# Performance work log

Hardware: AMD Instinct MI355X
Metric: run time of the kernel (lower is better)

## Reference

```python
import jax, jax.numpy as jnp
import numpy as np

R = 8921.0  # r defaults to n_labels[0] since args.r <= 0


def setup_inputs() -> dict:
    key = jax.random.key(0)
    k1, k2, k3 = jax.random.split(key, 3)
    B, S, D = 4, 4096, 512
    L = 8921  # n_labels (MIMIC-III full code set)
    x = jax.random.normal(k1, (B, S, D), dtype=jnp.float32)
    # Linear weights initialized N(0, 0.03) as in _init_weights
    W1 = jax.random.normal(k2, (D, D), dtype=jnp.float32) * 0.03  # first_linears[0]: size -> d_a
    W2 = jax.random.normal(k3, (L, D), dtype=jnp.float32) * 0.03  # second_linears[0]: d_a -> n_labels
    return {"x": x, "W1": W1, "W2": W2}


def reference(x, W1, W2):
    # weights = tanh(first_linear(x)) : [B, S, d_a]
    weights = jnp.tanh(jnp.einsum("bsd,ad->bsa", x, W1))
    # att scores: [B, S, L]; softmax over sequence dim (dim=1)
    att = jax.nn.softmax(jnp.einsum("bsa,la->bsl", weights, W2), axis=1)
    att_weights = jnp.swapaxes(att, 1, 2)  # [B, L, S]
    # weighted_output = att_weights @ x : [B, L, D]
    weighted = jnp.einsum("bls,bsd->bld", att_weights, x)
    # non-label attention_mode branch: sum over label dim / r
    out = jnp.sum(weighted, axis=1) / R  # [B, D]
    return (out, att_weights)
```

## Files before the change

kernel.cpp:

```cpp
#include <hip/hip_runtime.h>
#include <stdint.h>

typedef unsigned short u16;
typedef __bf16 bf16x8 __attribute__((ext_vector_type(8)));
typedef float f32x4 __attribute__((ext_vector_type(4)));

#define S_DIM 4096
#define D_DIM 512
#define B_DIM 4
#define L_DIM 8921
#define LPAD  8960
#define M1    16384

__device__ __forceinline__ u16 f2bf(float f) {
  uint32_t u = __float_as_uint(f);
  u += 0x7FFFu + ((u >> 16) & 1u);
  return (u16)(u >> 16);
}
__device__ __forceinline__ float bf2f(u16 u) {
  return __uint_as_float(((uint32_t)u) << 16);
}
__device__ __forceinline__ void async16(const u16* g, u16* l) {
  __builtin_amdgcn_global_load_lds((const __attribute__((address_space(1))) void*)g,
                                   (__attribute__((address_space(3))) void*)l, 16, 0, 0);
}

__global__ __launch_bounds__(256) void cast_pad_kernel(const float* __restrict__ src,
                                                       u16* __restrict__ dst,
                                                       long long nsrc, long long ndst) {
  long long i = ((long long)blockIdx.x * 256 + threadIdx.x) * 4;
  if (i >= ndst) return;
  ushort4 o;
  if (i < nsrc) {
    float4 v = *(const float4*)(src + i);
    o.x = f2bf(v.x); o.y = f2bf(v.y); o.z = f2bf(v.z); o.w = f2bf(v.w);
  } else {
    o.x = 0; o.y = 0; o.z = 0; o.w = 0;
  }
  *(ushort4*)(dst + i) = o;
}

__device__ __forceinline__ void gemm_core(const u16* __restrict__ A, const u16* __restrict__ B,
                                          int tileM, int tileN, u16* Al, u16* Bl,
                                          f32x4 acc[4][4], int waveM, int waveN,
                                          int quad, int l16) {
  const int t = threadIdx.x;
  const int r0 = t >> 2, c0 = (t & 3) * 8;
  for (int k0 = 0; k0 < D_DIM; k0 += 32) {
    async16(A + (size_t)(tileM + r0) * D_DIM + k0 + c0,        Al + t * 8);
    async16(A + (size_t)(tileM + r0 + 64) * D_DIM + k0 + c0,   Al + (t + 256) * 8);
    async16(B + (size_t)(tileN + r0) * D_DIM + k0 + c0,        Bl + t * 8);
    async16(B + (size_t)(tileN + r0 + 64) * D_DIM + k0 + c0,   Bl + (t + 256) * 8);
    __syncthreads();
    bf16x8 af[4], bfr[4];
#pragma unroll
    for (int mi = 0; mi < 4; ++mi)
      af[mi] = *(const bf16x8*)&Al[(waveM + mi * 16 + l16) * 32 + quad * 8];
#pragma unroll
    for (int ni = 0; ni < 4; ++ni)
      bfr[ni] = *(const bf16x8*)&Bl[(waveN + ni * 16 + l16) * 32 + quad * 8];
#pragma unroll
    for (int mi = 0; mi < 4; ++mi)
#pragma unroll
      for (int ni = 0; ni < 4; ++ni)
        acc[mi][ni] = __builtin_amdgcn_mfma_f32_16x16x32_bf16(af[mi], bfr[ni], acc[mi][ni], 0, 0, 0);
    __syncthreads();
  }
}

__global__ __launch_bounds__(256) void gemm1_tanh(const u16* __restrict__ A,
                                                  const u16* __restrict__ B,
                                                  u16* __restrict__ C) {
  __shared__ __align__(16) u16 Al[128 * 32];
  __shared__ __align__(16) u16 Bl[128 * 32];
  const int t = threadIdx.x, lane = t & 63, wave = t >> 6;
  const int quad = lane >> 4, l16 = lane & 15;
  const int tileM = blockIdx.y * 128, tileN = blockIdx.x * 128;
  const int waveM = (wave >> 1) * 64, waveN = (wave & 1) * 64;
  f32x4 acc[4][4];
  const f32x4 z = {0.f, 0.f, 0.f, 0.f};
#pragma unroll
  for (int mi = 0; mi < 4; ++mi)
#pragma unroll
    for (int ni = 0; ni < 4; ++ni) acc[mi][ni] = z;
  gemm_core(A, B, tileM, tileN, Al, Bl, acc, waveM, waveN, quad, l16);
#pragma unroll
  for (int mi = 0; mi < 4; ++mi) {
    const int m0 = tileM + waveM + mi * 16 + quad * 4;
#pragma unroll
    for (int ni = 0; ni < 4; ++ni) {
      const int n = tileN + waveN + ni * 16 + l16;
#pragma unroll
      for (int r = 0; r < 4; ++r)
        C[(size_t)(m0 + r) * D_DIM + n] = f2bf(tanhf(acc[mi][ni][r]));
    }
  }
}

template <bool BF16WS>
__global__ __launch_bounds__(256) void gemm2_exp(const u16* __restrict__ A,
                                                 const u16* __restrict__ Ball,
                                                 u16* __restrict__ scores,
                                                 float* __restrict__ attout,
                                                 float* __restrict__ rowsum) {
  __shared__ __align__(16) u16 Al[128 * 32];
  __shared__ __align__(16) u16 Bl[128 * 32];
  const int b = blockIdx.z;
  const u16* B = Ball + (size_t)b * S_DIM * D_DIM;
  const int t = threadIdx.x, lane = t & 63, wave = t >> 6;
  const int quad = lane >> 4, l16 = lane & 15;
  const int tileM = blockIdx.y * 128, tileN = blockIdx.x * 128;
  const int waveM = (wave >> 1) * 64, waveN = (wave & 1) * 64;
  f32x4 acc[4][4];
  const f32x4 z = {0.f, 0.f, 0.f, 0.f};
#pragma unroll
  for (int mi = 0; mi < 4; ++mi)
#pragma unroll
    for (int ni = 0; ni < 4; ++ni) acc[mi][ni] = z;
  gemm_core(A, B, tileM, tileN, Al, Bl, acc, waveM, waveN, quad, l16);

#pragma unroll
  for (int mi = 0; mi < 4; ++mi) {
    const int l0 = tileM + waveM + mi * 16 + quad * 4;
    float rs[4] = {0.f, 0.f, 0.f, 0.f};
#pragma unroll
    for (int ni = 0; ni < 4; ++ni) {
      const int s = tileN + waveN + ni * 16 + l16;
#pragma unroll
      for (int r = 0; r < 4; ++r) {
        const float ev = __expf(acc[mi][ni][r]);
        rs[r] += ev;
        const int l = l0 + r;
        if (l < L_DIM) {
          const size_t off = ((size_t)b * L_DIM + l) * S_DIM + s;
          if (BF16WS) scores[off] = f2bf(ev);
          else        attout[off] = ev;
        }
      }
    }
#pragma unroll
    for (int r = 0; r < 4; ++r) {
      float v = rs[r];
      v += __shfl_xor(v, 1);
      v += __shfl_xor(v, 2);
      v += __shfl_xor(v, 4);
      v += __shfl_xor(v, 8);
      if (l16 == 0) atomicAdd(&rowsum[(size_t)b * LPAD + l0 + r], v);
    }
  }
}

template <bool BF16WS>
__global__ __launch_bounds__(256) void normalize_colsum(const u16* __restrict__ scores,
                                                        const float* __restrict__ rowsum,
                                                        float* __restrict__ att,
                                                        float* __restrict__ colsum) {
  const int b = blockIdx.y;
  const int l0 = blockIdx.x * 32;
  const int t = threadIdx.x;
  __shared__ float sc[32];
  if (t < 32) {
    const int l = l0 + t;
    sc[t] = (l < L_DIM) ? 1.0f / rowsum[(size_t)b * LPAD + l] : 0.0f;
  }
  __syncthreads();
#pragma unroll
  for (int p = 0; p < 4; ++p) {
    const int s = p * 1024 + t * 4;
    float c0 = 0.f, c1 = 0.f, c2 = 0.f, c3 = 0.f;
    for (int i = 0; i < 32; ++i) {
      const int l = l0 + i;
      if (l >= L_DIM) break;
      const size_t off = ((size_t)b * L_DIM + l) * S_DIM + s;
      const float scale = sc[i];
      float v0, v1, v2, v3;
      if (BF16WS) {
        ushort4 u = *(const ushort4*)(scores + off);
        v0 = bf2f(u.x) * scale; v1 = bf2f(u.y) * scale;
        v2 = bf2f(u.z) * scale; v3 = bf2f(u.w) * scale;
      } else {
        float4 u = *(const float4*)(att + off);
        v0 = u.x * scale; v1 = u.y * scale; v2 = u.z * scale; v3 = u.w * scale;
      }
      float4 o = {v0, v1, v2, v3};
      *(float4*)(att + off) = o;
      c0 += v0; c1 += v1; c2 += v2; c3 += v3;
    }
    float* cs = colsum + (size_t)b * S_DIM + s;
    atomicAdd(cs + 0, c0); atomicAdd(cs + 1, c1);
    atomicAdd(cs + 2, c2); atomicAdd(cs + 3, c3);
  }
}

__global__ __launch_bounds__(256) void out_kernel(const float* __restrict__ x,
                                                  const float* __restrict__ colsum,
                                                  float* __restrict__ out) {
  const int b = blockIdx.y, s0 = blockIdx.x * 128, t = threadIdx.x;
  float a0 = 0.f, a1 = 0.f;
  for (int i = 0; i < 128; ++i) {
    const int s = s0 + i;
    const float c = colsum[(size_t)b * S_DIM + s];
    const float* xr = x + ((size_t)b * S_DIM + s) * D_DIM;
    a0 += c * xr[t];
    a1 += c * xr[t + 256];
  }
  const float invR = 1.0f / 8921.0f;
  atomicAdd(out + b * D_DIM + t,       a0 * invR);
  atomicAdd(out + b * D_DIM + t + 256, a1 * invR);
}

extern "C" void kernel_launch(void* const* d_in, const int* in_sizes, int n_in,
                              void* d_out, int out_size, void* d_ws, size_t ws_size,
                              hipStream_t stream) {
  const float* x  = (const float*)d_in[0];
  const float* W1 = (const float*)d_in[1];
  const float* W2 = (const float*)d_in[2];
  float* out = (float*)d_out;
  float* att = out + 2048;

  char* ws = (char*)d_ws;
  u16*   x_bf   = (u16*)(ws + 0);
  u16*   wt_bf  = (u16*)(ws + 16777216);
  u16*   w1_bf  = (u16*)(ws + 33554432);
  u16*   w2_bf  = (u16*)(ws + 34078720);
  float* rowsum = (float*)(ws + 43253760);
  float* colsum = (float*)(ws + 43397120);
  u16*   scores = (u16*)(ws + 43462656);
  const size_t need_big = 43462656ull + (size_t)B_DIM * L_DIM * S_DIM * 2ull;
  const bool big = ws_size >= need_big;

  hipMemsetAsync(rowsum, 0, (size_t)B_DIM * LPAD * 4, stream);
  hipMemsetAsync(colsum, 0, (size_t)B_DIM * S_DIM * 4, stream);
  hipMemsetAsync(out, 0, 2048 * sizeof(float), stream);

  cast_pad_kernel<<<8192, 256, 0, stream>>>(x,  x_bf,  8388608LL, 8388608LL);
  cast_pad_kernel<<<256,  256, 0, stream>>>(W1, w1_bf, 262144LL,  262144LL);
  cast_pad_kernel<<<4480, 256, 0, stream>>>(W2, w2_bf, (long long)L_DIM * 512, (long long)LPAD * 512);

  gemm1_tanh<<<dim3(4, 128), 256, 0, stream>>>(x_bf, w1_bf, wt_bf);

  dim3 g2(S_DIM / 128, LPAD / 128, B_DIM);
  if (big) {
    gemm2_exp<true><<<g2, 256, 0, stream>>>(w2_bf, wt_bf, scores, att, rowsum);
    normalize_colsum<true><<<dim3(279, 4), 256, 0, stream>>>(scores, rowsum, att, colsum);
  } else {
    gemm2_exp<false><<<g2, 256, 0, stream>>>(w2_bf, wt_bf, scores, att, rowsum);
    normalize_colsum<false><<<dim3(279, 4), 256, 0, stream>>>(scores, rowsum, att, colsum);
  }

  out_kernel<<<dim3(32, 4), 256, 0, stream>>>(x, colsum, out);
}
```

Measured before the change: 1.051 ms.

## Chunk label dimension so bf16 score staging fits any workspace size

Adds a chunked path that splits the label rows into pieces sized to the available workspace. For each piece, a GEMM+exp kernel writes bf16 exponentials and row sums into a small buffer, and a new 512-thread normalize kernel rescales them, writes fp32 attention, and accumulates column sums. This lets the bf16 intermediate be used even when the full buffer does not fit, and may keep chunks resident in cache. It also merges the two memsets into one and doubles out_kernel's grid. The cost is more kernel launches when the workspace is small.

```diff
diff --git a/kernel.cpp b/kernel.cpp
--- a/kernel.cpp
+++ b/kernel.cpp
@@ -4,6 +4,7 @@
 typedef unsigned short u16;
 typedef __bf16 bf16x8 __attribute__((ext_vector_type(8)));
 typedef float f32x4 __attribute__((ext_vector_type(4)));
+typedef unsigned short u16x8 __attribute__((ext_vector_type(8)));
 
 #define S_DIM 4096
 #define D_DIM 512
@@ -95,6 +96,97 @@
         C[(size_t)(m0 + r) * D_DIM + n] = f2bf(tanhf(acc[mi][ni][r]));
     }
   }
+}
+
+__global__ __launch_bounds__(256) void gemm2_exp_chunk(const u16* __restrict__ A,
+                                                       const u16* __restrict__ Ball,
+                                                       u16* __restrict__ scores,
+                                                       float* __restrict__ rowsum,
+                                                       int l_base, int lc_rows) {
+  __shared__ __align__(16) u16 Al[128 * 32];
+  __shared__ __align__(16) u16 Bl[128 * 32];
+  const int b = blockIdx.z;
+  const u16* B = Ball + (size_t)b * S_DIM * D_DIM;
+  const int t = threadIdx.x, lane = t & 63, wave = t >> 6;
+  const int quad = lane >> 4, l16 = lane & 15;
+  const int tileM = l_base + blockIdx.y * 128, tileN = blockIdx.x * 128;
+  const int waveM = (wave >> 1) * 64, waveN = (wave & 1) * 64;
+  f32x4 acc[4][4];
+  const f32x4 z = {0.f, 0.f, 0.f, 0.f};
+#pragma unroll
+  for (int mi = 0; mi < 4; ++mi)
+#pragma unroll
+    for (int ni = 0; ni < 4; ++ni) acc[mi][ni] = z;
+  gemm_core(A, B, tileM, tileN, Al, Bl, acc, waveM, waveN, quad, l16);
+
+#pragma unroll
+  for (int mi = 0; mi < 4; ++mi) {
+    const int l0 = tileM + waveM + mi * 16 + quad * 4;
+    float rs[4] = {0.f, 0.f, 0.f, 0.f};
+#pragma unroll
+    for (int ni = 0; ni < 4; ++ni) {
+      const int s = tileN + waveN + ni * 16 + l16;
+#pragma unroll
+      for (int r = 0; r < 4; ++r) {
+        const float ev = __expf(acc[mi][ni][r]);
+        rs[r] += ev;
+        const int l = l0 + r;
+        if (l < L_DIM) {
+          const size_t off = ((size_t)b * lc_rows + (l - l_base)) * S_DIM + s;
+          scores[off] = f2bf(ev);
+        }
+      }
+    }
+#pragma unroll
+    for (int r = 0; r < 4; ++r) {
+      float v = rs[r];
+      v += __shfl_xor(v, 1);
+      v += __shfl_xor(v, 2);
+      v += __shfl_xor(v, 4);
+      v += __shfl_xor(v, 8);
+      if (l16 == 0) atomicAdd(&rowsum[(size_t)b * LPAD + l0 + r], v);
+    }
+  }
+}
+
+__global__ __launch_bounds__(512) void normalize_colsum2(const u16* __restrict__ scores,
+                                                         const float* __restrict__ rowsum,
+                                                         float* __restrict__ att,
+                                                         float* __restrict__ colsum,
+                                                         int l_base, int lc_rows) {
+  const int b = blockIdx.y;
+  const int l0 = blockIdx.x * 64;
+  const int t = threadIdx.x;
+  const int s = t * 8;
+  __shared__ float sc[64];
+  if (t < 64) {
+    const int l = l_base + l0 + t;
+    sc[t] = (l < L_DIM) ? 1.0f / rowsum[(size_t)b * LPAD + l] : 0.0f;
+  }
+  __syncthreads();
+  float c0 = 0.f, c1 = 0.f, c2 = 0.f, c3 = 0.f, c4 = 0.f, c5 = 0.f, c6 = 0.f, c7 = 0.f;
+  int rmax = L_DIM - (l_base + l0);
+  if (rmax > 64) rmax = 64;
+  for (int i = 0; i < rmax; ++i) {
+    const size_t soff = ((size_t)b * lc_rows + l0 + i) * S_DIM + s;
+    u16x8 u = *(const u16x8*)(scores + soff);
+    const float sl = sc[i];
+    const float v0 = bf2f((u16)u[0]) * sl, v1 = bf2f((u16)u[1]) * sl;
+    const float v2 = bf2f((u16)u[2]) * sl, v3 = bf2f((u16)u[3]) * sl;
+    const float v4 = bf2f((u16)u[4]) * sl, v5 = bf2f((u16)u[5]) * sl;
+    const float v6 = bf2f((u16)u[6]) * sl, v7 = bf2f((u16)u[7]) * sl;
+    const size_t aoff = ((size_t)b * L_DIM + (l_base + l0 + i)) * S_DIM + s;
+    float4 w0 = {v0, v1, v2, v3}, w1 = {v4, v5, v6, v7};
+    *(float4*)(att + aoff)     = w0;
+    *(float4*)(att + aoff + 4) = w1;
+    c0 += v0; c1 += v1; c2 += v2; c3 += v3;
+    c4 += v4; c5 += v5; c6 += v6; c7 += v7;
+  }
+  float* cs = colsum + (size_t)b * S_DIM + s;
+  atomicAdd(cs + 0, c0); atomicAdd(cs + 1, c1);
+  atomicAdd(cs + 2, c2); atomicAdd(cs + 3, c3);
+  atomicAdd(cs + 4, c4); atomicAdd(cs + 5, c5);
+  atomicAdd(cs + 6, c6); atomicAdd(cs + 7, c7);
 }
 
 template <bool BF16WS>
@@ -118,7 +210,6 @@
 #pragma unroll
     for (int ni = 0; ni < 4; ++ni) acc[mi][ni] = z;
   gemm_core(A, B, tileM, tileN, Al, Bl, acc, waveM, waveN, quad, l16);
-
 #pragma unroll
   for (int mi = 0; mi < 4; ++mi) {
     const int l0 = tileM + waveM + mi * 16 + quad * 4;
@@ -195,9 +286,9 @@
 __global__ __launch_bounds__(256) void out_kernel(const float* __restrict__ x,
                                                   const float* __restrict__ colsum,
                                                   float* __restrict__ out) {
-  const int b = blockIdx.y, s0 = blockIdx.x * 128, t = threadIdx.x;
+  const int b = blockIdx.y, s0 = blockIdx.x * 64, t = threadIdx.x;
   float a0 = 0.f, a1 = 0.f;
-  for (int i = 0; i < 128; ++i) {
+  for (int i = 0; i < 64; ++i) {
     const int s = s0 + i;
     const float c = colsum[(size_t)b * S_DIM + s];
     const float* xr = x + ((size_t)b * S_DIM + s) * D_DIM;
@@ -226,11 +317,8 @@
   float* rowsum = (float*)(ws + 43253760);
   float* colsum = (float*)(ws + 43397120);
   u16*   scores = (u16*)(ws + 43462656);
-  const size_t need_big = 43462656ull + (size_t)B_DIM * L_DIM * S_DIM * 2ull;
-  const bool big = ws_size >= need_big;
-
-  hipMemsetAsync(rowsum, 0, (size_t)B_DIM * LPAD * 4, stream);
-  hipMemsetAsync(colsum, 0, (size_t)B_DIM * S_DIM * 4, stream);
+
+  hipMemsetAsync(rowsum, 0, (size_t)B_DIM * LPAD * 4 + (size_t)B_DIM * S_DIM * 4, stream);
   hipMemsetAsync(out, 0, 2048 * sizeof(float), stream);
 
   cast_pad_kernel<<<8192, 256, 0, stream>>>(x,  x_bf,  8388608LL, 8388608LL);
@@ -239,14 +327,27 @@
 
   gemm1_tanh<<<dim3(4, 128), 256, 0, stream>>>(x_bf, w1_bf, wt_bf);
 
-  dim3 g2(S_DIM / 128, LPAD / 128, B_DIM);
-  if (big) {
-    gemm2_exp<true><<<g2, 256, 0, stream>>>(w2_bf, wt_bf, scores, att, rowsum);
-    normalize_colsum<true><<<dim3(279, 4), 256, 0, stream>>>(scores, rowsum, att, colsum);
+  const size_t base = 43462656ull;
+  long long rows_fit = 0;
+  if (ws_size > base)
+    rows_fit = (long long)((ws_size - base) / ((size_t)B_DIM * S_DIM * 2));
+  rows_fit = (rows_fit / 128) * 128;
+
+  if (rows_fit >= 128) {
+    const int Lc = (int)(rows_fit < LPAD ? rows_fit : LPAD);
+    for (int lb = 0; lb < LPAD; lb += Lc) {
+      int rows = LPAD - lb;
+      if (rows > Lc) rows = Lc;
+      gemm2_exp_chunk<<<dim3(S_DIM / 128, rows / 128, B_DIM), 256, 0, stream>>>(
+          w2_bf, wt_bf, scores, rowsum, lb, rows);
+      normalize_colsum2<<<dim3(rows / 64, B_DIM), 512, 0, stream>>>(
+          scores, rowsum, att, colsum, lb, rows);
+    }
   } else {
-    gemm2_exp<false><<<g2, 256, 0, stream>>>(w2_bf, wt_bf, scores, att, rowsum);
-    normalize_colsum<false><<<dim3(279, 4), 256, 0, stream>>>(scores, rowsum, att, colsum);
-  }
-
-  out_kernel<<<dim3(32, 4), 256, 0, stream>>>(x, colsum, out);
-}
+    dim3 g2(S_DIM / 128, LPAD / 128, B_DIM);
+    gemm2_exp<false><<<g2, 256, 0, stream>>>(w2_bf, wt_bf, (u16*)nullptr, att, rowsum);
+    normalize_colsum<false><<<dim3(279, 4), 256, 0, stream>>>((const u16*)nullptr, rowsum, att, colsum);
+  }
+
+  out_kernel<<<dim3(64, 4), 256, 0, stream>>>(x, colsum, out);
+}
```

Result: no change. 1.040 ms (-1.0%).

## Recompute second GEMM instead of storing unnormalized scores to workspace

Applied to the files above, without the earlier changes.

Replaces the exp-write-then-normalize pass with two GEMM passes: the first only accumulates softmax row sums, the second recomputes the scores, normalizes them, writes the final attention and accumulates column sums in-register before issuing atomics. This removes the write and re-read of a large intermediate score tensor in exchange for doing the second GEMM twice. It also merges the two memsets into one and doubles the out_kernel grid.

```diff
diff --git a/kernel.cpp b/kernel.cpp
--- a/kernel.cpp
+++ b/kernel.cpp
@@ -16,9 +16,6 @@
   uint32_t u = __float_as_uint(f);
   u += 0x7FFFu + ((u >> 16) & 1u);
   return (u16)(u >> 16);
-}
-__device__ __forceinline__ float bf2f(u16 u) {
-  return __uint_as_float(((uint32_t)u) << 16);
 }
 __device__ __forceinline__ void async16(const u16* g, u16* l) {
   __builtin_amdgcn_global_load_lds((const __attribute__((address_space(1))) void*)g,
@@ -97,12 +94,9 @@
   }
 }
 
-template <bool BF16WS>
-__global__ __launch_bounds__(256) void gemm2_exp(const u16* __restrict__ A,
-                                                 const u16* __restrict__ Ball,
-                                                 u16* __restrict__ scores,
-                                                 float* __restrict__ attout,
-                                                 float* __restrict__ rowsum) {
+__global__ __launch_bounds__(256) void gemm2_rowsum(const u16* __restrict__ A,
+                                                    const u16* __restrict__ Ball,
+                                                    float* __restrict__ rowsum) {
   __shared__ __align__(16) u16 Al[128 * 32];
   __shared__ __align__(16) u16 Bl[128 * 32];
   const int b = blockIdx.z;
@@ -124,20 +118,10 @@
     const int l0 = tileM + waveM + mi * 16 + quad * 4;
     float rs[4] = {0.f, 0.f, 0.f, 0.f};
 #pragma unroll
-    for (int ni = 0; ni < 4; ++ni) {
-      const int s = tileN + waveN + ni * 16 + l16;
-#pragma unroll
-      for (int r = 0; r < 4; ++r) {
-        const float ev = __expf(acc[mi][ni][r]);
-        rs[r] += ev;
-        const int l = l0 + r;
-        if (l < L_DIM) {
-          const size_t off = ((size_t)b * L_DIM + l) * S_DIM + s;
-          if (BF16WS) scores[off] = f2bf(ev);
-          else        attout[off] = ev;
-        }
-      }
-    }
+    for (int ni = 0; ni < 4; ++ni)
+#pragma unroll
+      for (int r = 0; r < 4; ++r)
+        rs[r] += __expf(acc[mi][ni][r]);
 #pragma unroll
     for (int r = 0; r < 4; ++r) {
       float v = rs[r];
@@ -150,54 +134,68 @@
   }
 }
 
-template <bool BF16WS>
-__global__ __launch_bounds__(256) void normalize_colsum(const u16* __restrict__ scores,
-                                                        const float* __restrict__ rowsum,
-                                                        float* __restrict__ att,
-                                                        float* __restrict__ colsum) {
-  const int b = blockIdx.y;
-  const int l0 = blockIdx.x * 32;
-  const int t = threadIdx.x;
-  __shared__ float sc[32];
-  if (t < 32) {
-    const int l = l0 + t;
-    sc[t] = (l < L_DIM) ? 1.0f / rowsum[(size_t)b * LPAD + l] : 0.0f;
-  }
-  __syncthreads();
-#pragma unroll
-  for (int p = 0; p < 4; ++p) {
-    const int s = p * 1024 + t * 4;
-    float c0 = 0.f, c1 = 0.f, c2 = 0.f, c3 = 0.f;
-    for (int i = 0; i < 32; ++i) {
-      const int l = l0 + i;
-      if (l >= L_DIM) break;
-      const size_t off = ((size_t)b * L_DIM + l) * S_DIM + s;
-      const float scale = sc[i];
-      float v0, v1, v2, v3;
-      if (BF16WS) {
-        ushort4 u = *(const ushort4*)(scores + off);
-        v0 = bf2f(u.x) * scale; v1 = bf2f(u.y) * scale;
-        v2 = bf2f(u.z) * scale; v3 = bf2f(u.w) * scale;
-      } else {
-        float4 u = *(const float4*)(att + off);
-        v0 = u.x * scale; v1 = u.y * scale; v2 = u.z * scale; v3 = u.w * scale;
+__global__ __launch_bounds__(256) void gemm2_att(const u16* __restrict__ A,
+                                                 const u16* __restrict__ Ball,
+                                                 const float* __restrict__ rowsum,
+                                                 float* __restrict__ att,
+                                                 float* __restrict__ colsum) {
+  __shared__ __align__(16) u16 Al[128 * 32];
+  __shared__ __align__(16) u16 Bl[128 * 32];
+  const int b = blockIdx.z;
+  const u16* B = Ball + (size_t)b * S_DIM * D_DIM;
+  const int t = threadIdx.x, lane = t & 63, wave = t >> 6;
+  const int quad = lane >> 4, l16 = lane & 15;
+  const int tileM = blockIdx.y * 128, tileN = blockIdx.x * 128;
+  const int waveM = (wave >> 1) * 64, waveN = (wave & 1) * 64;
+  f32x4 acc[4][4];
+  const f32x4 z = {0.f, 0.f, 0.f, 0.f};
+#pragma unroll
+  for (int mi = 0; mi < 4; ++mi)
+#pragma unroll
+    for (int ni = 0; ni < 4; ++ni) acc[mi][ni] = z;
+  gemm_core(A, B, tileM, tileN, Al, Bl, acc, waveM, waveN, quad, l16);
+
+  float cs[4] = {0.f, 0.f, 0.f, 0.f};
+#pragma unroll
+  for (int mi = 0; mi < 4; ++mi) {
+    const int l0 = tileM + waveM + mi * 16 + quad * 4;
+    float inv[4];
+#pragma unroll
+    for (int r = 0; r < 4; ++r) {
+      const int l = l0 + r;
+      inv[r] = (l < L_DIM) ? 1.0f / rowsum[(size_t)b * LPAD + l] : 0.0f;
+    }
+#pragma unroll
+    for (int ni = 0; ni < 4; ++ni) {
+      const int s = tileN + waveN + ni * 16 + l16;
+#pragma unroll
+      for (int r = 0; r < 4; ++r) {
+        const float v = __expf(acc[mi][ni][r]) * inv[r];
+        cs[ni] += v;
+        const int l = l0 + r;
+        if (l < L_DIM)
+          att[((size_t)b * L_DIM + l) * S_DIM + s] = v;
       }
-      float4 o = {v0, v1, v2, v3};
-      *(float4*)(att + off) = o;
-      c0 += v0; c1 += v1; c2 += v2; c3 += v3;
-    }
-    float* cs = colsum + (size_t)b * S_DIM + s;
-    atomicAdd(cs + 0, c0); atomicAdd(cs + 1, c1);
-    atomicAdd(cs + 2, c2); atomicAdd(cs + 3, c3);
+    }
+  }
+#pragma unroll
+  for (int ni = 0; ni < 4; ++ni) {
+    float v = cs[ni];
+    v += __shfl_xor(v, 16);
+    v += __shfl_xor(v, 32);
+    if (quad == 0) {
+      const int s = tileN + waveN + ni * 16 + l16;
+      atomicAdd(&colsum[(size_t)b * S_DIM + s], v);
+    }
   }
 }
 
 __global__ __launch_bounds__(256) void out_kernel(const float* __restrict__ x,
                                                   const float* __restrict__ colsum,
                                                   float* __restrict__ out) {
-  const int b = blockIdx.y, s0 = blockIdx.x * 128, t = threadIdx.x;
+  const int b = blockIdx.y, s0 = blockIdx.x * 64, t = threadIdx.x;
   float a0 = 0.f, a1 = 0.f;
-  for (int i = 0; i < 128; ++i) {
+  for (int i = 0; i < 64; ++i) {
     const int s = s0 + i;
     const float c = colsum[(size_t)b * S_DIM + s];
     const float* xr = x + ((size_t)b * S_DIM + s) * D_DIM;
@@ -225,12 +223,8 @@
   u16*   w2_bf  = (u16*)(ws + 34078720);
   float* rowsum = (float*)(ws + 43253760);
   float* colsum = (float*)(ws + 43397120);
-  u16*   scores = (u16*)(ws + 43462656);
-  const size_t need_big = 43462656ull + (size_t)B_DIM * L_DIM * S_DIM * 2ull;
-  const bool big = ws_size >= need_big;
-
-  hipMemsetAsync(rowsum, 0, (size_t)B_DIM * LPAD * 4, stream);
-  hipMemsetAsync(colsum, 0, (size_t)B_DIM * S_DIM * 4, stream);
+
+  hipMemsetAsync(rowsum, 0, (size_t)B_DIM * LPAD * 4 + (size_t)B_DIM * S_DIM * 4, stream);
   hipMemsetAsync(out, 0, 2048 * sizeof(float), stream);
 
   cast_pad_kernel<<<8192, 256, 0, stream>>>(x,  x_bf,  8388608LL, 8388608LL);
@@ -239,14 +233,9 @@
 
   gemm1_tanh<<<dim3(4, 128), 256, 0, stream>>>(x_bf, w1_bf, wt_bf);
 
-  dim3 g2(S_DIM / 128, LPAD / 128, B_DIM);
-  if (big) {
-    gemm2_exp<true><<<g2, 256, 0, stream>>>(w2_bf, wt_bf, scores, att, rowsum);
-    normalize_colsum<true><<<dim3(279, 4), 256, 0, stream>>>(scores, rowsum, att, colsum);
-  } else {
-    gemm2_exp<false><<<g2, 256, 0, stream>>>(w2_bf, wt_bf, scores, att, rowsum);
-    normalize_colsum<false><<<dim3(279, 4), 256, 0, stream>>>(scores, rowsum, att, colsum);
-  }
-
-  out_kernel<<<dim3(32, 4), 256, 0, stream>>>(x, colsum, out);
-}
+  const dim3 g2(S_DIM / 128, LPAD / 128, B_DIM);
+  gemm2_rowsum<<<g2, 256, 0, stream>>>(w2_bf, wt_bf, rowsum);
+  gemm2_att  <<<g2, 256, 0, stream>>>(w2_bf, wt_bf, rowsum, att, colsum);
+
+  out_kernel<<<dim3(64, 4), 256, 0, stream>>>(x, colsum, out);
+}
```

New measurement: 991.6 us. 5.6% less time.
